# Kernel optimization log

Hardware: AMD Instinct MI355X
Metric: run time of the kernel (lower is better)

Reference implementation:

```python
import jax, jax.numpy as jnp
import numpy as np

N_NODES = 32768   # sum nodes in this partition
N_CHS = 32        # padded fan-in (power of 2)
MAX_ELS = 65536   # ch_prod_layer_size
B = 128           # batch
N_PARAMS = N_NODES * N_CHS
MIN_PROB = 1e-10


def setup_inputs() -> dict:
    key = jax.random.key(0)
    k1, k2, k3, k4 = jax.random.split(key, 4)
    node_mars = jnp.zeros((N_NODES, B), dtype=jnp.float32)
    element_mars = jax.random.normal(k1, (MAX_ELS, B), dtype=jnp.float32)
    params = jax.random.uniform(k2, (N_PARAMS,), dtype=jnp.float32)
    nids = jnp.arange(N_NODES, dtype=jnp.int64)
    cids = jax.random.randint(k3, (N_NODES, N_CHS), 0, MAX_ELS, dtype=jnp.int64)
    pids = jax.random.randint(k4, (N_NODES, N_CHS), 0, N_PARAMS, dtype=jnp.int64)
    return {"node_mars": node_mars, "element_mars": element_mars,
            "params": params, "nids": nids, "cids": cids, "pids": pids}


def reference(node_mars, element_mars, params, nids, cids, pids):
    # Gather child log-marginals: [N, C, B]
    ch_mars = element_mars[cids]
    # Stable weighted log-sum-exp over the child dim (dim=1), exactly as in
    # the SumLayer docstring:
    #   node_mars[nids] = log(clamp(sum(exp(ch - max) * params[pids]), 1e-10)) + max
    maxval = jnp.max(ch_mars, axis=1, keepdims=True)           # [N, 1, B]
    w = params[pids][:, :, None]                                # [N, C, 1]
    s = jnp.sum(jnp.exp(ch_mars - maxval) * w, axis=1)          # [N, B]
    vals = jnp.log(jnp.clip(s, MIN_PROB, None)) + maxval[:, 0, :]
    return node_mars.at[nids].set(vals)
```

## Files before the change

kernel.cpp:

```cpp
#include <hip/hip_runtime.h>
#include <math.h>


#define N_CHS 32
#define BATCH 128
#define N_ELS 65536

typedef float v2f __attribute__((ext_vector_type(2)));

__global__ __launch_bounds__(256) void exp_fp8_kernel(
    const float* __restrict__ em, unsigned int* __restrict__ y)
{
    const int i0 = blockIdx.x * 1024 + threadIdx.x;
    #pragma unroll
    for (int k = 0; k < 4; ++k) {
        const int i = i0 + k * 256;
        const float4 f = ((const float4*)em)[i];
        const float e0 = __expf(f.x), e1 = __expf(f.y);
        const float e2 = __expf(f.z), e3 = __expf(f.w);
        int w = 0;
        w = __builtin_amdgcn_cvt_pk_fp8_f32(e0, e1, w, false);
        w = __builtin_amdgcn_cvt_pk_fp8_f32(e2, e3, w, true);
        y[i] = (unsigned int)w;
    }
}

constexpr int TPN8 = 32;
constexpr int NPB8 = 8;
constexpr int BLOCK8 = TPN8 * NPB8;

__global__ __launch_bounds__(BLOCK8, 8) void sumlayer_fp8_kernel(
    const unsigned int* __restrict__ y,
    const float* __restrict__ params,
    const int*   __restrict__ nids,
    const int*   __restrict__ cids,
    const int*   __restrict__ pids,
    float*       __restrict__ out)
{
    __shared__ int   s_cid[BLOCK8];
    __shared__ float s_w[BLOCK8];

    const int tid   = threadIdx.x;
    const int node0 = blockIdx.x * NPB8;

    {
        const int g = node0 * N_CHS + tid;
        s_cid[tid] = cids[g];
        s_w[tid]   = params[pids[g]];
    }
    __syncthreads();

    const int nl = tid >> 5;
    const int b4 = tid & 31;
    const int n  = node0 + nl;

    float s0 = 0.0f, s1 = 0.0f, s2 = 0.0f, s3 = 0.0f;
    #pragma unroll
    for (int c = 0; c < N_CHS; ++c) {
        const unsigned int u = y[(size_t)s_cid[(nl << 5) + c] * TPN8 + b4];
        const float w = s_w[(nl << 5) + c];
        const v2f lo = __builtin_amdgcn_cvt_pk_f32_fp8(u, false);
        const v2f hi = __builtin_amdgcn_cvt_pk_f32_fp8(u, true);
        s0 = fmaf(lo.x, w, s0);
        s1 = fmaf(lo.y, w, s1);
        s2 = fmaf(hi.x, w, s2);
        s3 = fmaf(hi.y, w, s3);
    }

    float4 r;
    r.x = __logf(fmaxf(s0, 1e-30f));
    r.y = __logf(fmaxf(s1, 1e-30f));
    r.z = __logf(fmaxf(s2, 1e-30f));
    r.w = __logf(fmaxf(s3, 1e-30f));

    const int row = nids[n];
    ((float4*)out)[(size_t)row * TPN8 + b4] = r;
}

constexpr int NODES_PER_BLOCK = 4;
constexpr int THREADS_PER_NODE = 64;
constexpr int BLOCK = NODES_PER_BLOCK * THREADS_PER_NODE;

__global__ __launch_bounds__(BLOCK, 8) void sumlayer_fp32_kernel(
    const float* __restrict__ element_mars,
    const float* __restrict__ params,
    const int*   __restrict__ nids,
    const int*   __restrict__ cids,
    const int*   __restrict__ pids,
    float*       __restrict__ out)
{
    __shared__ int   s_cid[NODES_PER_BLOCK][N_CHS];
    __shared__ float s_w[NODES_PER_BLOCK][N_CHS];

    const int tid   = threadIdx.x;
    const int node0 = blockIdx.x * NODES_PER_BLOCK;

    if (tid < NODES_PER_BLOCK * N_CHS) {
        const int nl = tid >> 5;
        const int c  = tid & 31;
        const int g  = (node0 + nl) * N_CHS + c;
        s_cid[nl][c] = cids[g];
        s_w[nl][c]   = params[pids[g]];
    }
    __syncthreads();

    const int nl = tid / THREADS_PER_NODE;
    const int b2 = tid % THREADS_PER_NODE;
    const int n  = node0 + nl;
    const float2* em2 = (const float2*)element_mars;

    float sx0 = 0.0f, sx1 = 0.0f, sy0 = 0.0f, sy1 = 0.0f;
    #pragma unroll
    for (int c = 0; c < N_CHS; c += 2) {
        const float2 va = em2[(size_t)s_cid[nl][c]     * (BATCH / 2) + b2];
        const float2 vb = em2[(size_t)s_cid[nl][c + 1] * (BATCH / 2) + b2];
        const float wa = s_w[nl][c];
        const float wb = s_w[nl][c + 1];
        sx0 = fmaf(__expf(va.x), wa, sx0);
        sy0 = fmaf(__expf(va.y), wa, sy0);
        sx1 = fmaf(__expf(vb.x), wb, sx1);
        sy1 = fmaf(__expf(vb.y), wb, sy1);
    }

    float2 r;
    r.x = __logf(fmaxf(sx0 + sx1, 1e-30f));
    r.y = __logf(fmaxf(sy0 + sy1, 1e-30f));

    const int row = nids[n];
    ((float2*)out)[(size_t)row * (BATCH / 2) + b2] = r;
}

extern "C" void kernel_launch(void* const* d_in, const int* in_sizes, int n_in,
                              void* d_out, int out_size, void* d_ws, size_t ws_size,
                              hipStream_t stream) {
    const float* element_mars = (const float*)d_in[1];
    const float* params       = (const float*)d_in[2];
    const int*   nids         = (const int*)d_in[3];
    const int*   cids         = (const int*)d_in[4];
    const int*   pids         = (const int*)d_in[5];
    float*       out          = (float*)d_out;

    const int n_nodes = in_sizes[3];
    const size_t y_bytes = (size_t)N_ELS * BATCH;

    if (ws_size >= y_bytes) {
        unsigned int* y = (unsigned int*)d_ws;
        exp_fp8_kernel<<<2048, 256, 0, stream>>>(element_mars, y);
        sumlayer_fp8_kernel<<<n_nodes / NPB8, BLOCK8, 0, stream>>>(
            y, params, nids, cids, pids, out);
    } else {
        sumlayer_fp32_kernel<<<n_nodes / NODES_PER_BLOCK, BLOCK, 0, stream>>>(
            element_mars, params, nids, cids, pids, out);
    }
}
```

Measured before the change: 122.4 us.

## Fuse exp-to-fp8 pass and gather-sum into one cooperative kernel with grid sync

Replaces the two-kernel sequence (exp+fp8 pack, then gathered weighted sum) with a single cooperative launch of 1024 blocks. Each block first converts its slice of element_mars to fp8, then a grid-wide sync, then processes 32 nodes in four rounds. This removes one kernel launch boundary and the tail/ramp between kernels, at the cost of grid-sync overhead and lower parallelism in the gather phase (fixed 1024 blocks, looping over rounds). The fallback two-kernel path is kept if the cooperative launch fails.

```diff
diff --git a/kernel.cpp b/kernel.cpp
--- a/kernel.cpp
+++ b/kernel.cpp
@@ -1,5 +1,8 @@
 #include <hip/hip_runtime.h>
+#include <hip/hip_cooperative_groups.h>
 #include <math.h>
+
+namespace cg = cooperative_groups;
 
 
 #define N_CHS 32
@@ -8,21 +11,87 @@
 
 typedef float v2f __attribute__((ext_vector_type(2)));
 
+constexpr int COOP_GRID  = 1024;
+constexpr int COOP_BLOCK = 256;
+
+__global__ __launch_bounds__(COOP_BLOCK, 4) void sumlayer_fused_kernel(
+    const float* __restrict__ em,
+    unsigned int* __restrict__ y,
+    const float* __restrict__ params,
+    const int*   __restrict__ nids,
+    const int*   __restrict__ cids,
+    const int*   __restrict__ pids,
+    float*       __restrict__ out)
+{
+    const int tid = threadIdx.x;
+
+    {
+        const float4* em4 = (const float4*)em;
+        const int base = blockIdx.x * (8 * COOP_BLOCK);
+        #pragma unroll
+        for (int k = 0; k < 8; ++k) {
+            const int i = base + k * COOP_BLOCK + tid;
+            const float4 f = em4[i];
+            int w = 0;
+            w = __builtin_amdgcn_cvt_pk_fp8_f32(__expf(f.x), __expf(f.y), w, false);
+            w = __builtin_amdgcn_cvt_pk_fp8_f32(__expf(f.z), __expf(f.w), w, true);
+            y[i] = (unsigned int)w;
+        }
+    }
+
+    cg::this_grid().sync();
+
+    __shared__ int   s_cid[COOP_BLOCK];
+    __shared__ float s_w[COOP_BLOCK];
+
+    const int nl = tid >> 5;
+    const int b4 = tid & 31;
+
+    for (int r = 0; r < 4; ++r) {
+        const int node0 = blockIdx.x * 32 + r * 8;
+
+        {
+            const int g = node0 * N_CHS + tid;
+            s_cid[tid] = cids[g];
+            s_w[tid]   = params[pids[g]];
+        }
+        __syncthreads();
+
+        float s0 = 0.0f, s1 = 0.0f, s2 = 0.0f, s3 = 0.0f;
+        #pragma unroll
+        for (int c = 0; c < N_CHS; ++c) {
+            const unsigned int u = y[(size_t)s_cid[(nl << 5) + c] * 32 + b4];
+            const float w = s_w[(nl << 5) + c];
+            const v2f lo = __builtin_amdgcn_cvt_pk_f32_fp8(u, false);
+            const v2f hi = __builtin_amdgcn_cvt_pk_f32_fp8(u, true);
+            s0 = fmaf(lo.x, w, s0);
+            s1 = fmaf(lo.y, w, s1);
+            s2 = fmaf(hi.x, w, s2);
+            s3 = fmaf(hi.y, w, s3);
+        }
+
+        float4 rr;
+        rr.x = __logf(fmaxf(s0, 1e-30f));
+        rr.y = __logf(fmaxf(s1, 1e-30f));
+        rr.z = __logf(fmaxf(s2, 1e-30f));
+        rr.w = __logf(fmaxf(s3, 1e-30f));
+
+        const int row = nids[node0 + nl];
+        ((float4*)out)[(size_t)row * 32 + b4] = rr;
+
+        __syncthreads();
+    }
+}
+
 __global__ __launch_bounds__(256) void exp_fp8_kernel(
     const float* __restrict__ em, unsigned int* __restrict__ y)
 {
-    const int i0 = blockIdx.x * 1024 + threadIdx.x;
-    #pragma unroll
-    for (int k = 0; k < 4; ++k) {
-        const int i = i0 + k * 256;
-        const float4 f = ((const float4*)em)[i];
-        const float e0 = __expf(f.x), e1 = __expf(f.y);
-        const float e2 = __expf(f.z), e3 = __expf(f.w);
-        int w = 0;
-        w = __builtin_amdgcn_cvt_pk_fp8_f32(e0, e1, w, false);
-        w = __builtin_amdgcn_cvt_pk_fp8_f32(e2, e3, w, true);
-        y[i] = (unsigned int)w;
-    }
+    const int i = blockIdx.x * 256 + threadIdx.x;
+    const float4 f = ((const float4*)em)[i];
+    int w = 0;
+    w = __builtin_amdgcn_cvt_pk_fp8_f32(__expf(f.x), __expf(f.y), w, false);
+    w = __builtin_amdgcn_cvt_pk_fp8_f32(__expf(f.z), __expf(f.w), w, true);
+    y[i] = (unsigned int)w;
 }
 
 constexpr int TPN8 = 32;
@@ -145,9 +214,21 @@
 
     if (ws_size >= y_bytes) {
         unsigned int* y = (unsigned int*)d_ws;
-        exp_fp8_kernel<<<2048, 256, 0, stream>>>(element_mars, y);
-        sumlayer_fp8_kernel<<<n_nodes / NPB8, BLOCK8, 0, stream>>>(
-            y, params, nids, cids, pids, out);
+
+        void* args[] = {
+            (void*)&element_mars, (void*)&y, (void*)&params,
+            (void*)&nids, (void*)&cids, (void*)&pids, (void*)&out
+        };
+        hipError_t err = hipLaunchCooperativeKernel(
+            (const void*)sumlayer_fused_kernel,
+            dim3(COOP_GRID), dim3(COOP_BLOCK), args, 0, stream);
+
+        if (err != hipSuccess) {
+            const int n_f4 = N_ELS * BATCH / 4;
+            exp_fp8_kernel<<<n_f4 / 256, 256, 0, stream>>>(element_mars, y);
+            sumlayer_fp8_kernel<<<n_nodes / NPB8, BLOCK8, 0, stream>>>(
+                y, params, nids, cids, pids, out);
+        }
     } else {
         sumlayer_fp32_kernel<<<n_nodes / NODES_PER_BLOCK, BLOCK, 0, stream>>>(
             element_mars, params, nids, cids, pids, out);
```

After: 231.7 us. 89.2% more time.
